# Performance work log

Hardware: AMD Instinct MI355X
Metric: run time of the kernel (lower is better)

Reference implementation:

```python
import jax, jax.numpy as jnp
import numpy as np

B, L, E, H = 8, 1024, 768, 12
D = E // H  # 64 head dim


def _layernorm(x, scale, bias, eps=1e-6):
    m = jnp.mean(x, axis=-1, keepdims=True)
    v = jnp.var(x, axis=-1, keepdims=True)
    return (x - m) * jax.lax.rsqrt(v + eps) * scale + bias


def setup_inputs() -> dict:
    key = jax.random.key(0)
    ks = jax.random.split(key, 8)
    s = lambda fan_in: 1.0 / np.sqrt(fan_in)  # lecun-normal-ish init scale
    return {
        "x": jax.random.normal(ks[0], (B, L, E), jnp.float32),
        "ln1_scale": jnp.ones((E,), jnp.float32),
        "ln1_bias": jnp.zeros((E,), jnp.float32),
        "w_qkv": jax.random.normal(ks[1], (E, 3 * E), jnp.float32) * s(E),
        "b_qkv": jnp.zeros((3 * E,), jnp.float32),
        "w_proj": jax.random.normal(ks[2], (E, E), jnp.float32) * s(E),
        "b_proj": jnp.zeros((E,), jnp.float32),
        "ln2_scale": jnp.ones((E,), jnp.float32),
        "ln2_bias": jnp.zeros((E,), jnp.float32),
        "w_fc": jax.random.normal(ks[3], (E, 4 * E), jnp.float32) * s(E),
        "b_fc": jnp.zeros((4 * E,), jnp.float32),
        "w_out": jax.random.normal(ks[4], (4 * E, E), jnp.float32) * s(4 * E),
        "b_out": jnp.zeros((E,), jnp.float32),
    }


def reference(x, ln1_scale, ln1_bias, w_qkv, b_qkv, w_proj, b_proj,
              ln2_scale, ln2_bias, w_fc, b_fc, w_out, b_out):
    # eval mode: train=False (all dropouts are identity), mask_len=None
    b, l, _ = x.shape
    # ---- pre-LN causal self-attention ----
    z = _layernorm(x, ln1_scale, ln1_bias)
    qkv = z @ w_qkv + b_qkv                                   # (B, L, 3E)
    # faithful to source: reshape to (B, L, H, 3D) then split last axis
    qkv = qkv.reshape(b, l, H, 3 * D).transpose(0, 2, 1, 3)   # (B, H, L, 3D)
    q, k, v = jnp.split(qkv, 3, axis=-1)                      # each (B, H, L, D)
    attn = jnp.einsum("bhqd,bhkd->bhqk", q, k) / jnp.sqrt(jnp.float32(D))
    mask = jnp.tri(l, dtype=jnp.float32)                      # causal lower-tri
    attn = jnp.where(mask == 0, -1e18, attn)
    attn = jax.nn.softmax(attn, axis=-1)
    y = jnp.einsum("bhqk,bhkd->bhqd", attn, v)                # (B, H, L, D)
    y = y.transpose(0, 2, 1, 3).reshape(b, l, E)
    y = y @ w_proj + b_proj
    x = x + y  # residual (resid dropout is identity in eval)
    # ---- MLP block ----
    z = _layernorm(x, ln2_scale, ln2_bias)
    z = jax.nn.selu(z @ w_fc + b_fc) @ w_out + b_out
    return x + z
```

## Files before the change

### kernel.cpp

```cpp
#include <hip/hip_runtime.h>
#include <hip/hip_bf16.h>

typedef __attribute__((ext_vector_type(8))) short short8;
typedef __attribute__((ext_vector_type(4))) float f32x4;
typedef __attribute__((ext_vector_type(4))) unsigned short us4;

#define AS1 __attribute__((address_space(1)))
#define AS3 __attribute__((address_space(3)))

__device__ __forceinline__ unsigned short f2bf(float f) {
    unsigned u = __float_as_uint(f);
    u += 0x7fffu + ((u >> 16) & 1u);
    return (unsigned short)(u >> 16);
}

__device__ __forceinline__ void gload16(const void* g, void* l) {
    __builtin_amdgcn_global_load_lds((AS1 void*)(g), (AS3 void*)(l), 16, 0, 0);
}

__global__ __launch_bounds__(256) void prelude(const float* __restrict__ w_qkv,
                                               const float* __restrict__ w_proj,
                                               const float* __restrict__ w_fc,
                                               const float* __restrict__ w_out,
                                               unsigned short* __restrict__ wqkvT,
                                               unsigned short* __restrict__ wprojT,
                                               unsigned short* __restrict__ wfcT,
                                               unsigned short* __restrict__ woutT,
                                               const float* __restrict__ x,
                                               const float* __restrict__ sc,
                                               const float* __restrict__ bi,
                                               unsigned short* __restrict__ z) {
    __shared__ float tile[32][33];
    int id = blockIdx.x;
    if (id < 6912) {
        const float* in; unsigned short* out; int K, N, bn, bk;
        if (id < 1728)      {            in = w_qkv;  out = wqkvT;  K = 768;  N = 2304; bn = (id % 72) * 32; bk = (id / 72) * 32; }
        else if (id < 2304) { id -= 1728; in = w_proj; out = wprojT; K = 768;  N = 768;  bn = (id % 24) * 32; bk = (id / 24) * 32; }
        else if (id < 4608) { id -= 2304; in = w_fc;   out = wfcT;   K = 768;  N = 3072; bn = (id % 96) * 32; bk = (id / 96) * 32; }
        else                { id -= 4608; in = w_out;  out = woutT;  K = 3072; N = 768;  bn = (id % 24) * 32; bk = (id / 24) * 32; }
        int tx = threadIdx.x & 31, ty = threadIdx.x >> 5;
        #pragma unroll
        for (int i = ty; i < 32; i += 8)
            tile[i][tx] = in[(long)(bk + i) * N + bn + tx];
        __syncthreads();
        #pragma unroll
        for (int i = ty; i < 32; i += 8)
            out[(long)(bn + i) * K + bk + tx] = f2bf(tile[tx][i]);
    } else {
        long row = id - 6912;
        const float* xr = x + row * 768;
        int t = threadIdx.x;
        float v0 = xr[t], v1 = xr[t + 256], v2 = xr[t + 512];
        float s = v0 + v1 + v2;
        float ss = v0 * v0 + v1 * v1 + v2 * v2;
        #pragma unroll
        for (int m = 1; m < 64; m <<= 1) { s += __shfl_xor(s, m); ss += __shfl_xor(ss, m); }
        int wid = t >> 6;
        float* red = &tile[0][0];
        if ((t & 63) == 0) { red[wid] = s; red[4 + wid] = ss; }
        __syncthreads();
        s = red[0] + red[1] + red[2] + red[3];
        ss = red[4] + red[5] + red[6] + red[7];
        float mean = s * (1.f / 768.f);
        float var = fmaxf(ss * (1.f / 768.f) - mean * mean, 0.f);
        float rs = rsqrtf(var + 1e-6f);
        unsigned short* zr = z + row * 768;
        zr[t]       = f2bf((v0 - mean) * rs * sc[t]       + bi[t]);
        zr[t + 256] = f2bf((v1 - mean) * rs * sc[t + 256] + bi[t + 256]);
        zr[t + 512] = f2bf((v2 - mean) * rs * sc[t + 512] + bi[t + 512]);
    }
}

__global__ __launch_bounds__(256) void ln_row(const float* __restrict__ x,
                                              const float* __restrict__ sc,
                                              const float* __restrict__ bi,
                                              unsigned short* __restrict__ z) {
    long row = blockIdx.x;
    const float* xr = x + row * 768;
    int t = threadIdx.x;
    float v0 = xr[t], v1 = xr[t + 256], v2 = xr[t + 512];
    float s = v0 + v1 + v2;
    float ss = v0 * v0 + v1 * v1 + v2 * v2;
    #pragma unroll
    for (int m = 1; m < 64; m <<= 1) { s += __shfl_xor(s, m); ss += __shfl_xor(ss, m); }
    __shared__ float red[8];
    int wid = t >> 6;
    if ((t & 63) == 0) { red[wid] = s; red[4 + wid] = ss; }
    __syncthreads();
    s = red[0] + red[1] + red[2] + red[3];
    ss = red[4] + red[5] + red[6] + red[7];
    float mean = s * (1.f / 768.f);
    float var = fmaxf(ss * (1.f / 768.f) - mean * mean, 0.f);
    float rs = rsqrtf(var + 1e-6f);
    unsigned short* zr = z + row * 768;
    zr[t]       = f2bf((v0 - mean) * rs * sc[t]       + bi[t]);
    zr[t + 256] = f2bf((v1 - mean) * rs * sc[t + 256] + bi[t + 256]);
    zr[t + 512] = f2bf((v2 - mean) * rs * sc[t + 512] + bi[t + 512]);
}

template <int MODE>
__global__ __launch_bounds__(256, 2) void gemm_bf16(
    const unsigned short* __restrict__ A, const unsigned short* __restrict__ Bt,
    const float* __restrict__ bias, const float* __restrict__ resid,
    float* __restrict__ outf, unsigned short* __restrict__ outb,
    unsigned short* __restrict__ vt, int M, int N, int K) {
    __shared__ unsigned short As[128 * 64];
    __shared__ unsigned short Bs[128 * 64];
    const int tid = threadIdx.x, lane = tid & 63, wid = tid >> 6;
    const int wr = wid >> 1, wc = wid & 1;
    const int nwg = gridDim.x * gridDim.y;
    const int orig = blockIdx.y * gridDim.x + blockIdx.x;
    const int swz = (orig & 7) * (nwg >> 3) + (orig >> 3);
    const int bx = swz % gridDim.x, by = swz / gridDim.x;
    const long row0 = (long)by * 128, col0 = (long)bx * 128;

    f32x4 acc[4][4] = {};
    const int nkt = K >> 6;
    for (int t = 0; t < nkt; ++t) {
        #pragma unroll
        for (int kq = 0; kq < 4; kq++) {
            int U = kq * 256 + tid;
            int r = U >> 3, ch = U & 7;
            int kb = (ch * 16) ^ ((r & 7) << 4);
            gload16(A + (row0 + r) * K + t * 64 + (kb >> 1), &As[(kq * 256 + wid * 64) * 8]);
            gload16(Bt + (col0 + r) * K + t * 64 + (kb >> 1), &Bs[(kq * 256 + wid * 64) * 8]);
        }
        __syncthreads();
        #pragma unroll
        for (int kk = 0; kk < 2; kk++) {
            short8 af[4], bf[4];
            #pragma unroll
            for (int m = 0; m < 4; m++) {
                int r = wr * 64 + m * 16 + (lane & 15);
                int off = r * 128 + ((kk * 64 + ((lane >> 4) * 16)) ^ ((r & 7) << 4));
                af[m] = *(const short8*)((const char*)As + off);
            }
            #pragma unroll
            for (int n = 0; n < 4; n++) {
                int r = wc * 64 + n * 16 + (lane & 15);
                int off = r * 128 + ((kk * 64 + ((lane >> 4) * 16)) ^ ((r & 7) << 4));
                bf[n] = *(const short8*)((const char*)Bs + off);
            }
            #pragma unroll
            for (int m = 0; m < 4; m++)
                #pragma unroll
                for (int n = 0; n < 4; n++)
                    acc[m][n] = __builtin_amdgcn_mfma_f32_16x16x32_bf16(af[m], bf[n], acc[m][n], 0, 0, 0);
        }
        __syncthreads();
    }

    const float LAM = 1.0507009873554805f, LAMAL = 1.7580993408473766f;
    #pragma unroll
    for (int n = 0; n < 4; n++) {
        int c = (int)col0 + wc * 64 + n * 16 + (lane & 15);
        float bv = bias[c];
        #pragma unroll
        for (int m = 0; m < 4; m++) {
            long r0 = row0 + wr * 64 + m * 16 + ((lane >> 4) * 4);
            f32x4 v = acc[m][n];
            v += bv;
            if (MODE == 0) {
                int h = c / 192, rem = c - h * 192;
                if (rem < 128) {
                    #pragma unroll
                    for (int r = 0; r < 4; r++) outb[(r0 + r) * 2304 + c] = f2bf(v[r]);
                } else {
                    int d = rem - 128;
                    long bb = r0 >> 10, l = r0 & 1023;
                    us4 p;
                    #pragma unroll
                    for (int r = 0; r < 4; r++) p[r] = f2bf(v[r]);
                    *(us4*)(vt + ((bb * 12 + h) * 64 + d) * 1024 + l) = p;
                }
            } else if (MODE == 1) {
                #pragma unroll
                for (int r = 0; r < 4; r++)
                    outf[(r0 + r) * (long)N + c] = v[r] + resid[(r0 + r) * (long)N + c];
            } else if (MODE == 2) {
                #pragma unroll
                for (int r = 0; r < 4; r++) {
                    float s = v[r];
                    s = s > 0.f ? LAM * s : LAMAL * (__expf(s) - 1.f);
                    outb[(r0 + r) * (long)N + c] = f2bf(s);
                }
            }
        }
    }
}

__global__ __launch_bounds__(256, 2) void attn_kernel(const unsigned short* __restrict__ qkv,
                                                      const unsigned short* __restrict__ vt,
                                                      unsigned short* __restrict__ y) {
    __shared__ unsigned short Kd[2][64 * 64];
    __shared__ unsigned short Vd[2][64 * 64];
    __shared__ unsigned short Ps[4][32 * 64];
    const int tid = threadIdx.x, lane = tid & 63, wid = tid >> 6;
    const int bh = blockIdx.x;
    const int qt = 7 - (int)blockIdx.y;
    const int b = bh / 12, h = bh - b * 12;
    const unsigned short* kptr = qkv + (long)b * 1024 * 2304 + h * 192 + 64;
    const unsigned short* vptr = vt + (long)bh * 64 * 1024;
    const long qrow0 = (long)b * 1024 + qt * 128;

    auto stageKV = [&](int buf, int kvt) {
        #pragma unroll
        for (int kq = 0; kq < 2; kq++) {
            int U = kq * 256 + tid;
            int r = U >> 3, ch = U & 7;
            int kb = (ch * 16) ^ ((r & 7) << 4);
            gload16(kptr + (long)(kvt * 64 + r) * 2304 + (kb >> 1), &Kd[buf][(kq * 256 + wid * 64) * 8]);
            gload16(vptr + (long)r * 1024 + kvt * 64 + (kb >> 1), &Vd[buf][(kq * 256 + wid * 64) * 8]);
        }
    };

    unsigned short* Qs = &Ps[0][0];
    const unsigned short* qptr = qkv + qrow0 * 2304 + h * 192;
    #pragma unroll
    for (int kq = 0; kq < 4; kq++) {
        int U = kq * 256 + tid;
        int r = U >> 3, ch = U & 7;
        int kb = (ch * 16) ^ ((r & 7) << 4);
        gload16(qptr + (long)r * 2304 + (kb >> 1), &Qs[(kq * 256 + wid * 64) * 8]);
    }
    stageKV(0, 0);
    asm volatile("s_waitcnt vmcnt(0)" ::: "memory");
    __builtin_amdgcn_s_barrier();
    short8 qf[2][2];
    #pragma unroll
    for (int m = 0; m < 2; m++)
        #pragma unroll
        for (int kk = 0; kk < 2; kk++) {
            int r = wid * 32 + m * 16 + (lane & 15);
            int off = r * 128 + ((kk * 64 + ((lane >> 4) * 16)) ^ ((r & 7) << 4));
            qf[m][kk] = *(const short8*)((const char*)Qs + off);
        }

    f32x4 O[2][4] = {};
    float mrow[2][4], lrow[2][4];
    #pragma unroll
    for (int m = 0; m < 2; m++)
        #pragma unroll
        for (int r = 0; r < 4; r++) { mrow[m][r] = -3.0e38f; lrow[m][r] = 0.f; }

    const int qlo = qt * 128 + wid * 32;
    const int nkv = (qt + 1) * 2;

    for (int kvt = 0; kvt < nkv; ++kvt) {
        const int cur = kvt & 1;
        const bool pf = (kvt + 1 < nkv);
        if (pf) stageKV(cur ^ 1, kvt + 1);
        if (pf) asm volatile("s_waitcnt vmcnt(4)" ::: "memory");
        else    asm volatile("s_waitcnt vmcnt(0)" ::: "memory");
        __builtin_amdgcn_s_barrier();
        if (kvt * 64 <= qlo + 31) {
            const unsigned short* Ks = &Kd[cur][0];
            const unsigned short* Vs = &Vd[cur][0];
            f32x4 s[2][4] = {};
            #pragma unroll
            for (int kk = 0; kk < 2; kk++) {
                short8 kf[4];
                #pragma unroll
                for (int n = 0; n < 4; n++) {
                    int r = n * 16 + (lane & 15);
                    int off = r * 128 + ((kk * 64 + ((lane >> 4) * 16)) ^ ((r & 7) << 4));
                    kf[n] = *(const short8*)((const char*)Ks + off);
                }
                #pragma unroll
                for (int m = 0; m < 2; m++)
                    #pragma unroll
                    for (int n = 0; n < 4; n++)
                        s[m][n] = __builtin_amdgcn_mfma_f32_16x16x32_bf16(qf[m][kk], kf[n], s[m][n], 0, 0, 0);
            }
            const bool needmask = (kvt * 64 + 63) > qlo;
            #pragma unroll
            for (int m = 0; m < 2; m++)
                #pragma unroll
                for (int n = 0; n < 4; n++) {
                    s[m][n] = s[m][n] * 0.125f;
                    if (needmask) {
                        int c = kvt * 64 + n * 16 + (lane & 15);
                        #pragma unroll
                        for (int r = 0; r < 4; r++) {
                            int rr = qlo + m * 16 + ((lane >> 4) * 4) + r;
                            if (c > rr) s[m][n][r] = -1.0e30f;
                        }
                    }
                }
            #pragma unroll
            for (int m = 0; m < 2; m++)
                #pragma unroll
                for (int r = 0; r < 4; r++) {
                    float mx = fmaxf(fmaxf(s[m][0][r], s[m][1][r]), fmaxf(s[m][2][r], s[m][3][r]));
                    #pragma unroll
                    for (int msk = 1; msk < 16; msk <<= 1) mx = fmaxf(mx, __shfl_xor(mx, msk));
                    float mnew = fmaxf(mrow[m][r], mx);
                    float al = __expf(mrow[m][r] - mnew);
                    float ps = 0.f;
                    #pragma unroll
                    for (int n = 0; n < 4; n++) {
                        float p = __expf(s[m][n][r] - mnew);
                        s[m][n][r] = p;
                        ps += p;
                    }
                    #pragma unroll
                    for (int msk = 1; msk < 16; msk <<= 1) ps += __shfl_xor(ps, msk);
                    lrow[m][r] = lrow[m][r] * al + ps;
                    mrow[m][r] = mnew;
                    #pragma unroll
                    for (int n = 0; n < 4; n++) O[m][n][r] *= al;
                }
            unsigned short* pw = Ps[wid];
            #pragma unroll
            for (int m = 0; m < 2; m++)
                #pragma unroll
                for (int n = 0; n < 4; n++)
                    #pragma unroll
                    for (int r = 0; r < 4; r++) {
                        int pr = m * 16 + ((lane >> 4) * 4) + r;
                        int off = (pr * 128 + (n * 16 + (lane & 15)) * 2) ^ ((pr & 7) << 4);
                        *(unsigned short*)((char*)pw + off) = f2bf(s[m][n][r]);
                    }
            #pragma unroll
            for (int kk = 0; kk < 2; kk++) {
                short8 pf2[2], vf[4];
                #pragma unroll
                for (int m = 0; m < 2; m++) {
                    int r = m * 16 + (lane & 15);
                    int off = r * 128 + ((kk * 64 + ((lane >> 4) * 16)) ^ ((r & 7) << 4));
                    pf2[m] = *(const short8*)((const char*)pw + off);
                }
                #pragma unroll
                for (int n = 0; n < 4; n++) {
                    int r = n * 16 + (lane & 15);
                    int off = r * 128 + ((kk * 64 + ((lane >> 4) * 16)) ^ ((r & 7) << 4));
                    vf[n] = *(const short8*)((const char*)Vs + off);
                }
                #pragma unroll
                for (int m = 0; m < 2; m++)
                    #pragma unroll
                    for (int n = 0; n < 4; n++)
                        O[m][n] = __builtin_amdgcn_mfma_f32_16x16x32_bf16(pf2[m], vf[n], O[m][n], 0, 0, 0);
            }
        }
        __builtin_amdgcn_s_barrier();
    }
    unsigned short* yb = y + (qrow0 + wid * 32) * 768 + h * 64;
    #pragma unroll
    for (int m = 0; m < 2; m++)
        #pragma unroll
        for (int n = 0; n < 4; n++)
            #pragma unroll
            for (int r = 0; r < 4; r++) {
                int rr = m * 16 + ((lane >> 4) * 4) + r;
                yb[(long)rr * 768 + n * 16 + (lane & 15)] = f2bf(O[m][n][r] / lrow[m][r]);
            }
}

extern "C" void kernel_launch(void* const* d_in, const int* in_sizes, int n_in,
                              void* d_out, int out_size, void* d_ws, size_t ws_size,
                              hipStream_t stream) {
    (void)in_sizes; (void)n_in; (void)out_size; (void)ws_size;
    const float* x      = (const float*)d_in[0];
    const float* ln1_s  = (const float*)d_in[1];
    const float* ln1_b  = (const float*)d_in[2];
    const float* w_qkv  = (const float*)d_in[3];
    const float* b_qkv  = (const float*)d_in[4];
    const float* w_proj = (const float*)d_in[5];
    const float* b_proj = (const float*)d_in[6];
    const float* ln2_s  = (const float*)d_in[7];
    const float* ln2_b  = (const float*)d_in[8];
    const float* w_fc   = (const float*)d_in[9];
    const float* b_fc   = (const float*)d_in[10];
    const float* w_out  = (const float*)d_in[11];
    const float* b_out  = (const float*)d_in[12];

    unsigned short* wqkvT = (unsigned short*)d_ws;
    unsigned short* wprojT = wqkvT + (size_t)2304 * 768;
    unsigned short* wfcT   = wprojT + (size_t)768 * 768;
    unsigned short* woutT  = wfcT + (size_t)3072 * 768;
    unsigned short* zbuf   = woutT + (size_t)768 * 3072;
    unsigned short* qkvb   = zbuf + (size_t)8192 * 768;
    unsigned short* vtb    = qkvb + (size_t)8192 * 2304;
    unsigned short* abuf   = qkvb;
    float* x2 = (float*)(vtb + (size_t)96 * 64 * 1024);

    prelude<<<15104, 256, 0, stream>>>(w_qkv, w_proj, w_fc, w_out, wqkvT, wprojT, wfcT, woutT,
                                       x, ln1_s, ln1_b, zbuf);
    gemm_bf16<0><<<dim3(18, 64), 256, 0, stream>>>(zbuf, wqkvT, b_qkv, nullptr, nullptr, qkvb, vtb, 8192, 2304, 768);
    attn_kernel<<<dim3(96, 8), 256, 0, stream>>>(qkvb, vtb, zbuf);
    gemm_bf16<1><<<dim3(6, 64), 256, 0, stream>>>(zbuf, wprojT, b_proj, x, x2, nullptr, nullptr, 8192, 768, 768);
    ln_row<<<8192, 256, 0, stream>>>(x2, ln2_s, ln2_b, zbuf);
    gemm_bf16<2><<<dim3(24, 64), 256, 0, stream>>>(zbuf, wfcT, b_fc, nullptr, nullptr, abuf, nullptr, 8192, 3072, 768);
    gemm_bf16<1><<<dim3(6, 64), 256, 0, stream>>>(abuf, woutT, b_out, x2, (float*)d_out, nullptr, nullptr, 8192, 768, 3072);
}
```

Before: 364.3 us.

## Double-buffer GEMM LDS tiles and use narrower N tiles for E-output GEMMs

The GEMM kernel now keeps two LDS buffers. It issues the global-to-LDS loads for the next K tile before computing the current one, and waits with explicit vmcnt counts in place of a full syncthreads, so loads overlap MFMA work. A BN template parameter is added, and the two GEMMs with 768 output columns use 64-wide N tiles. This doubles their grid from 384 to 768 blocks so the GPU's compute units are better filled. The cost is twice the LDS per block and reliance on hand-counted waitcnt values being correct.

Result: faster. 355.8 us (-2.4%).

```diff
diff --git a/kernel.cpp b/kernel.cpp
--- a/kernel.cpp
+++ b/kernel.cpp
@@ -98,62 +98,81 @@
     zr[t + 512] = f2bf((v2 - mean) * rs * sc[t + 512] + bi[t + 512]);
 }
 
-template <int MODE>
-__global__ __launch_bounds__(256, 2) void gemm_bf16(
+template <int MODE, int BN>
+__global__ __launch_bounds__(256, (BN == 64 ? 3 : 2)) void gemm_bf16(
     const unsigned short* __restrict__ A, const unsigned short* __restrict__ Bt,
     const float* __restrict__ bias, const float* __restrict__ resid,
     float* __restrict__ outf, unsigned short* __restrict__ outb,
     unsigned short* __restrict__ vt, int M, int N, int K) {
-    __shared__ unsigned short As[128 * 64];
-    __shared__ unsigned short Bs[128 * 64];
+    constexpr int NFRN = BN / 32;
+    __shared__ unsigned short As[2][128 * 64];
+    __shared__ unsigned short Bs[2][BN * 64];
     const int tid = threadIdx.x, lane = tid & 63, wid = tid >> 6;
     const int wr = wid >> 1, wc = wid & 1;
     const int nwg = gridDim.x * gridDim.y;
     const int orig = blockIdx.y * gridDim.x + blockIdx.x;
     const int swz = (orig & 7) * (nwg >> 3) + (orig >> 3);
     const int bx = swz % gridDim.x, by = swz / gridDim.x;
-    const long row0 = (long)by * 128, col0 = (long)bx * 128;
-
-    f32x4 acc[4][4] = {};
-    const int nkt = K >> 6;
-    for (int t = 0; t < nkt; ++t) {
+    const long row0 = (long)by * 128, col0 = (long)bx * BN;
+
+    auto stage = [&](int buf, int t) {
         #pragma unroll
         for (int kq = 0; kq < 4; kq++) {
             int U = kq * 256 + tid;
             int r = U >> 3, ch = U & 7;
             int kb = (ch * 16) ^ ((r & 7) << 4);
-            gload16(A + (row0 + r) * K + t * 64 + (kb >> 1), &As[(kq * 256 + wid * 64) * 8]);
-            gload16(Bt + (col0 + r) * K + t * 64 + (kb >> 1), &Bs[(kq * 256 + wid * 64) * 8]);
-        }
-        __syncthreads();
+            gload16(A + (row0 + r) * K + (long)t * 64 + (kb >> 1), &As[buf][(kq * 256 + wid * 64) * 8]);
+        }
+        #pragma unroll
+        for (int kq = 0; kq < BN / 32; kq++) {
+            int U = kq * 256 + tid;
+            int r = U >> 3, ch = U & 7;
+            int kb = (ch * 16) ^ ((r & 7) << 4);
+            gload16(Bt + (col0 + r) * K + (long)t * 64 + (kb >> 1), &Bs[buf][(kq * 256 + wid * 64) * 8]);
+        }
+    };
+
+    f32x4 acc[4][NFRN] = {};
+    const int nkt = K >> 6;
+    stage(0, 0);
+    for (int t = 0; t < nkt; ++t) {
+        const int cur = t & 1;
+        if (t + 1 < nkt) {
+            stage(cur ^ 1, t + 1);
+            if constexpr (BN == 128) asm volatile("s_waitcnt vmcnt(8)" ::: "memory");
+            else                     asm volatile("s_waitcnt vmcnt(6)" ::: "memory");
+        } else {
+            asm volatile("s_waitcnt vmcnt(0)" ::: "memory");
+        }
+        __builtin_amdgcn_s_barrier();
         #pragma unroll
         for (int kk = 0; kk < 2; kk++) {
-            short8 af[4], bf[4];
+            short8 af[4], bf[NFRN];
             #pragma unroll
             for (int m = 0; m < 4; m++) {
                 int r = wr * 64 + m * 16 + (lane & 15);
                 int off = r * 128 + ((kk * 64 + ((lane >> 4) * 16)) ^ ((r & 7) << 4));
-                af[m] = *(const short8*)((const char*)As + off);
-            }
-            #pragma unroll
-            for (int n = 0; n < 4; n++) {
-                int r = wc * 64 + n * 16 + (lane & 15);
+                af[m] = *(const short8*)((const char*)&As[cur][0] + off);
+            }
+            #pragma unroll
+            for (int n = 0; n < NFRN; n++) {
+                int r = wc * (BN / 2) + n * 16 + (lane & 15);
                 int off = r * 128 + ((kk * 64 + ((lane >> 4) * 16)) ^ ((r & 7) << 4));
-                bf[n] = *(const short8*)((const char*)Bs + off);
+                bf[n] = *(const short8*)((const char*)&Bs[cur][0] + off);
             }
             #pragma unroll
             for (int m = 0; m < 4; m++)
                 #pragma unroll
-                for (int n = 0; n < 4; n++)
+                for (int n = 0; n < NFRN; n++)
                     acc[m][n] = __builtin_amdgcn_mfma_f32_16x16x32_bf16(af[m], bf[n], acc[m][n], 0, 0, 0);
         }
-        __syncthreads();
+        __builtin_amdgcn_s_barrier();
     }
 
     const float LAM = 1.0507009873554805f, LAMAL = 1.7580993408473766f;
     #pragma unroll
-    for (int n = 0; n < 4; n++) {
-        int c = (int)col0 + wc * 64 + n * 16 + (lane & 15);
+    for (int n = 0; n < NFRN; n++) {
+        int c = (int)col0 + wc * (BN / 2) + n * 16 + (lane & 15);
         float bv = bias[c];
         #pragma unroll
         for (int m = 0; m < 4; m++) {
@@ -387,10 +406,10 @@
 
     prelude<<<15104, 256, 0, stream>>>(w_qkv, w_proj, w_fc, w_out, wqkvT, wprojT, wfcT, woutT,
                                        x, ln1_s, ln1_b, zbuf);
-    gemm_bf16<0><<<dim3(18, 64), 256, 0, stream>>>(zbuf, wqkvT, b_qkv, nullptr, nullptr, qkvb, vtb, 8192, 2304, 768);
+    gemm_bf16<0, 128><<<dim3(18, 64), 256, 0, stream>>>(zbuf, wqkvT, b_qkv, nullptr, nullptr, qkvb, vtb, 8192, 2304, 768);
     attn_kernel<<<dim3(96, 8), 256, 0, stream>>>(qkvb, vtb, zbuf);
-    gemm_bf16<1><<<dim3(6, 64), 256, 0, stream>>>(zbuf, wprojT, b_proj, x, x2, nullptr, nullptr, 8192, 768, 768);
+    gemm_bf16<1, 64><<<dim3(12, 64), 256, 0, stream>>>(zbuf, wprojT, b_proj, x, x2, nullptr, nullptr, 8192, 768, 768);
     ln_row<<<8192, 256, 0, stream>>>(x2, ln2_s, ln2_b, zbuf);
-    gemm_bf16<2><<<dim3(24, 64), 256, 0, stream>>>(zbuf, wfcT, b_fc, nullptr, nullptr, abuf, nullptr, 8192, 3072, 768);
-    gemm_bf16<1><<<dim3(6, 64), 256, 0, stream>>>(abuf, woutT, b_out, x2, (float*)d_out, nullptr, nullptr, 8192, 768, 3072);
-}
+    gemm_bf16<2, 128><<<dim3(24, 64), 256, 0, stream>>>(zbuf, wfcT, b_fc, nullptr, nullptr, abuf, nullptr, 8192, 3072, 768);
+    gemm_bf16<1, 64><<<dim3(12, 64), 256, 0, stream>>>(abuf, woutT, b_out, x2, (float*)d_out, nullptr, nullptr, 8192, 768, 3072);
+}
```
